# Kernel optimization log

Hardware: AMD Instinct MI355X
Metric: run time of the kernel (lower is better)

The kernel has to match this reference:

```python
import jax, jax.numpy as jnp
import numpy as np

B, H, W = 2, 512, 512
HID, NHKD, HEADS, KD, CD = 64, 128, 8, 16, 64
MAX_SHAPE = 512

def _conv(x, w, b=None, pad=0, groups=1):
    y = jax.lax.conv_general_dilated(x, w, (1, 1), [(pad, pad), (pad, pad)],
                                     dimension_numbers=('NCHW', 'OIHW', 'NCHW'),
                                     feature_group_count=groups)
    return y if b is None else y + b[None, :, None, None]

def _gelu(x):
    return jax.nn.gelu(x, approximate=False)  # torch nn.GELU default is exact erf

def _bn(x, s, t):
    # inference-mode BatchNorm folded to per-channel scale/shift
    return x * s[None, :, None, None] + t[None, :, None, None]

def _dyn_pos(xm, pe):
    # xm: (B, C, N); pe: (1, C, MAX_SHAPE); linear interp (align_corners=False) when N != MAX_SHAPE
    N = xm.shape[-1]
    if N != pe.shape[-1]:
        pe = jax.image.resize(pe, (1, pe.shape[1], N), method='linear')
    return xm + pe

def _sdpa(q, k, v):
    # q, k, v: (B, heads, L=key_dim, E=H); scale = 1/sqrt(E) as in F.scaled_dot_product_attention
    scale = 1.0 / np.sqrt(q.shape[-1])
    attn = jax.nn.softmax(jnp.einsum('bhie,bhje->bhij', q, k) * scale, axis=-1)
    return jnp.einsum('bhij,bhje->bhie', attn, v)

def setup_inputs():
    key = jax.random.key(0)
    ks = jax.random.split(key, 26)
    rn = lambda i, shp, sc=1.0: jax.random.normal(ks[i], shp, jnp.float32) * sc
    return {
        'x': rn(0, (B, HID, H, W)),
        'shortcut': rn(1, (B, CD, H, W)),
        'ln_w': jnp.ones((CD,), jnp.float32),
        'ln_b': jnp.zeros((CD,), jnp.float32),
        'dproj_dw_w': rn(2, (CD, 1, 3, 3), 0.2),
        'dproj_bn_s': 1.0 + rn(3, (CD,), 0.1),
        'dproj_bn_t': rn(4, (CD,), 0.1),
        'dproj_pw_w': rn(5, (2 * HID, CD, 1, 1), 0.125),
        'dproj_pw_b': rn(6, (2 * HID,), 0.05),
        'q_dw_w': rn(7, (NHKD, 1, 3, 3), 0.2),
        'q_bn_s': 1.0 + rn(8, (NHKD,), 0.1),
        'q_bn_t': rn(9, (NHKD,), 0.1),
        'k_dw_w': rn(10, (NHKD, 1, 3, 3), 0.2),
        'k_bn_s': 1.0 + rn(11, (NHKD,), 0.1),
        'k_bn_t': rn(12, (NHKD,), 0.1),
        'v_pw_w': rn(13, (NHKD, HID, 1, 1), 0.125),
        'v_bn_s': 1.0 + rn(14, (NHKD,), 0.1),
        'v_bn_t': rn(15, (NHKD,), 0.1),
        'proj_dw_w': rn(16, (HID + 2 * NHKD, 1, 3, 3), 0.2),
        'proj_dw_b': rn(17, (HID + 2 * NHKD,), 0.05),
        'proj_pw_w': rn(18, (HID, HID + 2 * NHKD, 1, 1), 0.06),
        'proj_pw_b': rn(19, (HID,), 0.05),
        'pe_rowq': rn(20, (1, NHKD, MAX_SHAPE), 0.02),
        'pe_rowk': rn(21, (1, NHKD, MAX_SHAPE), 0.02),
        'pe_colq': rn(22, (1, NHKD, MAX_SHAPE), 0.02),
        'pe_colk': rn(23, (1, NHKD, MAX_SHAPE), 0.02),
        'ape_row_w': jnp.ones((1, NHKD, 1, 1), jnp.float32),
        'ape_col_w': jnp.ones((1, NHKD, 1, 1), jnp.float32),
    }

def reference(x, shortcut, ln_w, ln_b, dproj_dw_w, dproj_bn_s, dproj_bn_t,
              dproj_pw_w, dproj_pw_b, q_dw_w, q_bn_s, q_bn_t, k_dw_w, k_bn_s,
              k_bn_t, v_pw_w, v_bn_s, v_bn_t, proj_dw_w, proj_dw_b, proj_pw_w,
              proj_pw_b, pe_rowq, pe_rowk, pe_colq, pe_colk, ape_row_w, ape_col_w):
    b, _, h, w = x.shape
    # LayerNorm2d: normalize over channel axis (biased variance, eps=1e-5)
    mu = shortcut.mean(axis=1, keepdims=True)
    var = shortcut.var(axis=1, keepdims=True)
    sn = (shortcut - mu) / jnp.sqrt(var + 1e-5) * ln_w[None, :, None, None] + ln_b[None, :, None, None]
    # d_proj: dw3x3 -> BN -> GELU -> pw1x1 -> GELU
    s = _gelu(_bn(_conv(sn, dproj_dw_w, pad=1, groups=CD), dproj_bn_s, dproj_bn_t))
    s = _gelu(_conv(s, dproj_pw_w, dproj_pw_b))
    k_in, v_in = jnp.split(s, 2, axis=1)  # each (B, HID, H, W)
    # q/k: grouped 3x3 conv (groups=HID, out=NHKD) -> BN -> GELU; v: 1x1 -> BN
    q = _gelu(_bn(_conv(x, q_dw_w, pad=1, groups=HID), q_bn_s, q_bn_t))
    k = _gelu(_bn(_conv(k_in, k_dw_w, pad=1, groups=HID), k_bn_s, k_bn_t))
    v = _bn(_conv(v_in, v_pw_w), v_bn_s, v_bn_t)
    # row attention: pool over W, seq dim = key_dim (16), head dim = H
    qr = _dyn_pos(q.mean(-1), pe_rowq).reshape(b, HEADS, KD, h)
    kr = _dyn_pos(k.mean(-1), pe_rowk).reshape(b, HEADS, KD, h)
    vr = v.mean(-1).reshape(b, HEADS, KD, h)
    attn_row = _sdpa(qr, kr, vr).reshape(b, NHKD, 1, h)
    # column attention: pool over H
    qc = _dyn_pos(q.mean(-2), pe_colq).reshape(b, HEADS, KD, w)
    kc = _dyn_pos(k.mean(-2), pe_colk).reshape(b, HEADS, KD, w)
    vc = v.mean(-2).reshape(b, HEADS, KD, w)
    attn_col = _sdpa(qc, kc, vc).reshape(b, NHKD, 1, w)
    # AxialPositionEncoding: both maps broadcast over spatial axis 2 (requires H == W)
    attn = v + ape_row_w * attn_row + ape_col_w * attn_col
    cat = jnp.concatenate([x, attn, v], axis=1)  # (B, 320, H, W)
    ctot = cat.shape[1]
    # channel shuffle: 'b (c g) h w -> b (g c) h w', g=5
    shuf = cat.reshape(b, ctot // 5, 5, h, w).transpose(0, 2, 1, 3, 4).reshape(b, ctot, h, w)
    p = _gelu(_conv(shuf, proj_dw_w, proj_dw_b, pad=1, groups=ctot))
    p = _conv(p, proj_pw_w, proj_pw_b)
    return _gelu(p)
```

## Files before the change

kernel.cpp:

```cpp
#include <hip/hip_runtime.h>
#include <math.h>

#define PLANE (512*512)

typedef short bf16x8 __attribute__((ext_vector_type(8)));
typedef float f32x4 __attribute__((ext_vector_type(4)));

__device__ __forceinline__ float gelu_f(float x) {
    float ax = fabsf(x) * 0.70710678118654752440f;
    float t = __builtin_amdgcn_rcpf(1.0f + 0.3275911f * ax);
    float poly = t * (0.254829592f + t * (-0.284496736f + t * (1.421413741f
               + t * (-1.453152027f + t * 1.061405429f))));
    float e = __expf(-ax * ax);
    float er = 1.0f - poly * e;
    er = copysignf(er, x);
    return 0.5f * x * (1.0f + er);
}

__device__ __forceinline__ unsigned short f2bf(float f) {
    union { float f; unsigned u; } v; v.f = f;
    unsigned r = v.u + 0x7FFFu + ((v.u >> 16) & 1u);
    return (unsigned short)(r >> 16);
}

__global__ __launch_bounds__(256) void k_lnstats(const float* __restrict__ sc,
                                                 float* __restrict__ Pb,
                                                 float* __restrict__ Qb) {
    int p = blockIdx.x * 256 + threadIdx.x;
    int b = p >> 18;
    int hw = p & (PLANE - 1);
    const float* src = sc + (size_t)b * 64 * PLANE + hw;
    float sum = 0.f, sq = 0.f;
    #pragma unroll 8
    for (int c = 0; c < 64; ++c) {
        float v = src[(size_t)c * PLANE];
        sum += v; sq += v * v;
    }
    float mu = sum * (1.0f / 64.0f);
    float var = sq * (1.0f / 64.0f) - mu * mu;
    float rstd = rsqrtf(var + 1e-5f);
    Pb[p] = rstd;
    Qb[p] = -mu * rstd;
}

__global__ __launch_bounds__(256) void k_dw64ln(const float* __restrict__ sc,
                                                const float* __restrict__ dww,
                                                const float* __restrict__ lnw,
                                                const float* __restrict__ lnb,
                                                const float* __restrict__ bns,
                                                const float* __restrict__ bnt,
                                                const float* __restrict__ Pb,
                                                const float* __restrict__ Qb,
                                                unsigned* __restrict__ t1b) {
    int p = blockIdx.x * 256 + threadIdx.x;
    int b = p >> 18;
    int hw = p & (PLANE - 1);
    int h = hw >> 9, w = hw & 511;
    int tapoff[9]; float Pt[9], Qt[9], vm[9];
    const float* Pp = Pb + (size_t)b * PLANE;
    const float* Qp = Qb + (size_t)b * PLANE;
    #pragma unroll
    for (int dh = -1; dh <= 1; ++dh)
        #pragma unroll
        for (int dw = -1; dw <= 1; ++dw) {
            int k = (dh + 1) * 3 + dw + 1;
            int hh = h + dh, ww = w + dw;
            bool ok = (hh >= 0 && hh < 512 && ww >= 0 && ww < 512);
            int hc = ok ? hh : h, wc = ok ? ww : w;
            int off = hc * 512 + wc;
            tapoff[k] = off;
            vm[k] = ok ? 1.f : 0.f;
            Pt[k] = Pp[off]; Qt[k] = Qp[off];
        }
    const float* scb = sc + (size_t)b * 64 * PLANE;
    unsigned* ob = t1b + (size_t)b * 32 * PLANE + hw;
    for (int c2 = 0; c2 < 32; ++c2) {
        float g[2];
        #pragma unroll
        for (int e = 0; e < 2; ++e) {
            int c = c2 * 2 + e;
            const float* wp = dww + c * 9;
            const float* cp = scb + (size_t)c * PLANE;
            float conv = 0.f, wsum = 0.f;
            #pragma unroll
            for (int k = 0; k < 9; ++k) {
                float wv = wp[k];
                float raw = cp[tapoff[k]];
                conv = fmaf(wv, fmaf(raw, Pt[k], Qt[k]) * vm[k], conv);
                wsum = fmaf(wv, vm[k], wsum);
            }
            float a = lnw[c] * conv + lnb[c] * wsum;
            g[e] = gelu_f(a * bns[c] + bnt[c]);
        }
        unsigned r;
        asm("v_cvt_pk_bf16_f32 %0,%1,%2" : "=v"(r) : "v"(g[0]), "v"(g[1]));
        ob[(size_t)c2 * PLANE] = r;
    }
}

__global__ __launch_bounds__(256) void k_wsetup2(const float* __restrict__ W1,
                                                 const float* __restrict__ W2,
                                                 unsigned short* __restrict__ w1b,
                                                 unsigned short* __restrict__ w2b) {
    int tid = blockIdx.x * 256 + threadIdx.x;
    if (tid < 8192) { w1b[tid] = f2bf(W1[tid]); w2b[tid] = f2bf(W2[tid]); }
}

__global__ __launch_bounds__(256, 4) void k_pw2(
    const unsigned* __restrict__ t1b,
    const unsigned short* __restrict__ w1b, const float* __restrict__ b1,
    const unsigned short* __restrict__ w2b,
    const float* __restrict__ vbs, const float* __restrict__ vbt,
    float* __restrict__ k_in, float* __restrict__ v)
{
    __shared__ unsigned short vin[64][88];
    __shared__ float epi[64 * 68];
    __shared__ float psl[128], ptl[128], pbl[128];
    int tid = threadIdx.x;
    if (tid < 128) { psl[tid] = vbs[tid]; ptl[tid] = vbt[tid]; pbl[tid] = b1[tid]; }
    int lane = tid & 63, wva = tid >> 6;
    int cl = lane & 15, kg = lane >> 4;
    int p0 = blockIdx.x * 64;
    int b = p0 >> 18;
    int hw0 = p0 & (PLANE - 1);
    int px = wva * 16 + cl;
    const unsigned* tp = t1b + (size_t)b * 32 * PLANE + hw0 + px;
    __syncthreads();

    unsigned bfr[2][4];
    #pragma unroll
    for (int ks = 0; ks < 2; ++ks)
        #pragma unroll
        for (int jp = 0; jp < 4; ++jp)
            bfr[ks][jp] = tp[(size_t)(ks * 16 + kg * 4 + jp) * PLANE];

    f32x4 acc[8];
    #pragma unroll
    for (int mt = 0; mt < 8; ++mt) acc[mt] = (f32x4){0.f, 0.f, 0.f, 0.f};
    #pragma unroll
    for (int ks = 0; ks < 2; ++ks) {
        union { unsigned u[4]; bf16x8 v; } bb;
        bb.u[0] = bfr[ks][0]; bb.u[1] = bfr[ks][1]; bb.u[2] = bfr[ks][2]; bb.u[3] = bfr[ks][3];
        #pragma unroll
        for (int mt = 0; mt < 8; ++mt) {
            bf16x8 af = *(const bf16x8*)(w1b + (size_t)(mt * 16 + cl) * 64 + ks * 32 + kg * 8);
            acc[mt] = __builtin_amdgcn_mfma_f32_16x16x32_bf16(af, bb.v, acc[mt], 0, 0, 0);
        }
    }

    #pragma unroll
    for (int mt = 4; mt < 8; ++mt) {
        float g[4];
        #pragma unroll
        for (int r = 0; r < 4; ++r)
            g[r] = gelu_f(acc[mt][r] + pbl[mt * 16 + kg * 4 + r]);
        unsigned r01, r23;
        asm("v_cvt_pk_bf16_f32 %0,%1,%2" : "=v"(r01) : "v"(g[0]), "v"(g[1]));
        asm("v_cvt_pk_bf16_f32 %0,%1,%2" : "=v"(r23) : "v"(g[2]), "v"(g[3]));
        int ch = (mt - 4) * 16 + kg * 4;
        *(unsigned*)&vin[px][ch]     = r01;
        *(unsigned*)&vin[px][ch + 2] = r23;
    }

    __syncthreads();
    #pragma unroll
    for (int mt = 0; mt < 4; ++mt)
        #pragma unroll
        for (int r = 0; r < 4; ++r) {
            int m = mt * 16 + kg * 4 + r;
            epi[m * 68 + px] = gelu_f(acc[mt][r] + pbl[m]);
        }
    __syncthreads();
    float* kb = k_in + (size_t)b * 64 * PLANE + hw0;
    #pragma unroll
    for (int k = 0; k < 4; ++k) {
        int m = wva * 16 + k * 4 + kg;
        float4 vv = *(const float4*)&epi[m * 68 + cl * 4];
        *(float4*)&kb[(size_t)m * PLANE + cl * 4] = vv;
    }

    f32x4 acc2[8];
    #pragma unroll
    for (int mt = 0; mt < 8; ++mt) acc2[mt] = (f32x4){0.f, 0.f, 0.f, 0.f};
    #pragma unroll
    for (int ks = 0; ks < 2; ++ks) {
        bf16x8 bb = *(const bf16x8*)&vin[px][ks * 32 + kg * 8];
        #pragma unroll
        for (int mt = 0; mt < 8; ++mt) {
            bf16x8 af = *(const bf16x8*)(w2b + (size_t)(mt * 16 + cl) * 64 + ks * 32 + kg * 8);
            acc2[mt] = __builtin_amdgcn_mfma_f32_16x16x32_bf16(af, bb, acc2[mt], 0, 0, 0);
        }
    }

    float* vb = v + (size_t)b * 128 * PLANE + hw0;
    #pragma unroll
    for (int pass = 0; pass < 2; ++pass) {
        __syncthreads();
        #pragma unroll
        for (int mt = pass * 4; mt < pass * 4 + 4; ++mt)
            #pragma unroll
            for (int r = 0; r < 4; ++r) {
                int m = mt * 16 + kg * 4 + r;
                epi[(m - pass * 64) * 68 + px] = acc2[mt][r] * psl[m] + ptl[m];
            }
        __syncthreads();
        #pragma unroll
        for (int k = 0; k < 4; ++k) {
            int ml = wva * 16 + k * 4 + kg;
            float4 vv = *(const float4*)&epi[ml * 68 + cl * 4];
            *(float4*)&vb[(size_t)(pass * 64 + ml) * PLANE + cl * 4] = vv;
        }
    }
}

__global__ __launch_bounds__(512) void k_dwpool(const float* __restrict__ in,
                                                const float* __restrict__ wt,
                                                const float* __restrict__ bns,
                                                const float* __restrict__ bnt,
                                                float* __restrict__ rowsum,
                                                float* __restrict__ colpart) {
    __shared__ float lred[2][8][8];
    int tid = threadIdx.x;
    int blk = blockIdx.x;
    int hc = blk & 63;
    int g  = (blk >> 6) & 63;
    int b  = blk >> 12;
    int o0 = 2 * g, o1 = 2 * g + 1;
    const float* ip = in + ((size_t)b * 64 + g) * PLANE;
    float w0[9], w1[9];
    #pragma unroll
    for (int k = 0; k < 9; ++k) { w0[k] = wt[o0 * 9 + k]; w1[k] = wt[o1 * 9 + k]; }
    float s0 = bns[o0], t0 = bnt[o0], s1 = bns[o1], tt1 = bnt[o1];
    int wx = tid;
    float ca0 = 0.f, ca1 = 0.f;
    int lane = tid & 63, wv = tid >> 6;
    for (int r = 0; r < 8; ++r) {
        int h = hc * 8 + r;
        float nb[9];
        #pragma unroll
        for (int dh = -1; dh <= 1; ++dh) {
            #pragma unroll
            for (int dw = -1; dw <= 1; ++dw) {
                int hh = h + dh, ww = wx + dw;
                nb[(dh + 1) * 3 + dw + 1] =
                    (hh >= 0 && hh < 512 && ww >= 0 && ww < 512) ? ip[hh * 512 + ww] : 0.f;
            }
        }
        float a0 = 0.f, a1 = 0.f;
        #pragma unroll
        for (int k = 0; k < 9; ++k) { a0 += w0[k] * nb[k]; a1 += w1[k] * nb[k]; }
        a0 = gelu_f(a0 * s0 + t0);
        a1 = gelu_f(a1 * s1 + tt1);
        ca0 += a0; ca1 += a1;
        #pragma unroll
        for (int off = 32; off > 0; off >>= 1) {
            a0 += __shfl_down(a0, off, 64);
            a1 += __shfl_down(a1, off, 64);
        }
        if (lane == 0) { lred[0][r][wv] = a0; lred[1][r][wv] = a1; }
    }
    colpart[(((size_t)b * 128 + o0) * 64 + hc) * 512 + wx] = ca0;
    colpart[(((size_t)b * 128 + o1) * 64 + hc) * 512 + wx] = ca1;
    __syncthreads();
    if (tid < 16) {
        int oo = tid >> 3, r = tid & 7;
        float s = 0.f;
        #pragma unroll
        for (int i = 0; i < 8; ++i) s += lred[oo][r][i];
        int och = oo == 0 ? o0 : o1;
        rowsum[((size_t)b * 128 + och) * 512 + hc * 8 + r] = s;
    }
}

__global__ __launch_bounds__(512) void k_vpool(const float* __restrict__ v,
                                               float* __restrict__ rowsum,
                                               float* __restrict__ colpart) {
    __shared__ float lred[8][8];
    int tid = threadIdx.x;
    int blk = blockIdx.x;
    int hc = blk & 63;
    int bc = blk >> 6;
    const float* ip = v + (size_t)bc * PLANE;
    float ca = 0.f;
    int lane = tid & 63, wv = tid >> 6;
    for (int r = 0; r < 8; ++r) {
        float a = ip[(hc * 8 + r) * 512 + tid];
        ca += a;
        #pragma unroll
        for (int off = 32; off > 0; off >>= 1) a += __shfl_down(a, off, 64);
        if (lane == 0) lred[r][wv] = a;
    }
    colpart[((size_t)bc * 64 + hc) * 512 + tid] = ca;
    __syncthreads();
    if (tid < 8) {
        float s = 0.f;
        #pragma unroll
        for (int i = 0; i < 8; ++i) s += lred[tid][i];
        rowsum[(size_t)bc * 512 + hc * 8 + tid] = s;
    }
}

__global__ __launch_bounds__(256) void k_colreduce(const float* __restrict__ part,
                                                   float* __restrict__ out, int n) {
    int idx = blockIdx.x * 256 + threadIdx.x;
    if (idx >= n) return;
    int bc = idx >> 9, w = idx & 511;
    const float* pp = part + ((size_t)bc * 64) * 512 + w;
    float s = 0.f;
    #pragma unroll
    for (int p = 0; p < 64; ++p) s += pp[p * 512];
    out[idx] = s;
}

__global__ __launch_bounds__(256) void k_attn(const float* __restrict__ qrow,
                                              const float* __restrict__ krow,
                                              const float* __restrict__ vrow,
                                              const float* __restrict__ qcol,
                                              const float* __restrict__ kcol,
                                              const float* __restrict__ vcol,
                                              const float* __restrict__ perq,
                                              const float* __restrict__ perk,
                                              const float* __restrict__ pecq,
                                              const float* __restrict__ peck,
                                              float* __restrict__ arow,
                                              float* __restrict__ acol) {
    __shared__ float P[16][17];
    int blk = blockIdx.x;
    int axis = blk & 1;
    int head = (blk >> 1) & 7;
    int b = blk >> 4;
    const float* qs = axis ? qcol : qrow;
    const float* ks = axis ? kcol : krow;
    const float* vs = axis ? vcol : vrow;
    const float* peq = axis ? pecq : perq;
    const float* pek = axis ? peck : perk;
    float* out = axis ? acol : arow;
    int tid = threadIdx.x;
    int i = tid >> 4, j = tid & 15;
    int ci = head * 16 + i, cj = head * 16 + j;
    const float* qp = qs + ((size_t)b * 128 + ci) * 512;
    const float* kp = ks + ((size_t)b * 128 + cj) * 512;
    const float* qe = peq + ci * 512;
    const float* ke = pek + cj * 512;
    float s = 0.f;
    for (int n = 0; n < 512; ++n) {
        float qv = qp[n] * (1.f / 512.f) + qe[n];
        float kv = kp[n] * (1.f / 512.f) + ke[n];
        s += qv * kv;
    }
    s *= 0.0441941738241592203f;
    P[i][j] = s;
    __syncthreads();
    if (tid < 16) {
        float mx = -1e30f;
        #pragma unroll
        for (int jj = 0; jj < 16; ++jj) mx = fmaxf(mx, P[tid][jj]);
        float e[16];
        float sum = 0.f;
        #pragma unroll
        for (int jj = 0; jj < 16; ++jj) { e[jj] = expf(P[tid][jj] - mx); sum += e[jj]; }
        float inv = 1.f / sum;
        #pragma unroll
        for (int jj = 0; jj < 16; ++jj) P[tid][jj] = e[jj] * inv;
    }
    __syncthreads();
    for (int idx = tid; idx < 16 * 512; idx += 256) {
        int ii = idx >> 9, n = idx & 511;
        const float* vb = vs + ((size_t)b * 128 + head * 16) * 512 + n;
        float acc = 0.f;
        #pragma unroll
        for (int jj = 0; jj < 16; ++jj) acc += P[ii][jj] * vb[jj * 512] * (1.f / 512.f);
        out[((size_t)b * 128 + head * 16 + ii) * 512 + n] = acc;
    }
}

__global__ __launch_bounds__(256) void k_wsetup(const float* __restrict__ pww,
                                                unsigned short* __restrict__ wsh) {
    int tid = blockIdx.x * 256 + threadIdx.x;
    if (tid >= 64 * 320) return;
    int m = tid / 320, src = tid % 320;
    int o = (src % 5) * 64 + src / 5;
    wsh[m * 320 + src] = f2bf(pww[m * 320 + o]);
}

__global__ __launch_bounds__(256) void k_awsetup(const float* __restrict__ pdw,
                                                 const float* __restrict__ aprw,
                                                 const float* __restrict__ apcw,
                                                 const float* __restrict__ arow,
                                                 const float* __restrict__ acol,
                                                 float* __restrict__ aw) {
    int idx = blockIdx.x * 256 + threadIdx.x;
    if (idx >= 2 * 128 * 512) return;
    int col = idx & 511;
    int c   = (idx >> 9) & 127;
    int b   = idx >> 16;
    int src = 64 + c;
    int o = (src % 5) * 64 + src / 5;
    const float* wd = pdw + o * 9;
    float ws0 = wd[0] + wd[3] + wd[6];
    float ws1 = wd[1] + wd[4] + wd[7];
    float ws2 = wd[2] + wd[5] + wd[8];
    const float* ar = arow + ((size_t)b * 128 + c) * 512;
    const float* ac = acol + ((size_t)b * 128 + c) * 512;
    float apr = aprw[c], apc = apcw[c];
    float sum = ws1 * (apr * ar[col] + apc * ac[col]);
    if (col > 0)   sum += ws0 * (apr * ar[col - 1] + apc * ac[col - 1]);
    if (col < 511) sum += ws2 * (apr * ar[col + 1] + apc * ac[col + 1]);
    aw[idx] = sum;
}

template<bool HE, bool WE>
__device__ __forceinline__ void conv2x2(const float* __restrict__ p,
    const float* wlA, const float* wlP,
    const int* hrow, const float* rv, int ls, int rs, float cv0, float cv2,
    float outA[2], float outP[2])
{
    float a0,a1,a2, b0,b1,b2, c0,c1,c2;
    const float* q = p + hrow[0]*512;
    if (WE) { a0=q[ls]*cv0; a1=q[0]; a2=q[rs]*cv2; } else { a0=q[-1]; a1=q[0]; a2=q[1]; }
    q = p + hrow[1]*512;
    if (WE) { b0=q[ls]*cv0; b1=q[0]; b2=q[rs]*cv2; } else { b0=q[-1]; b1=q[0]; b2=q[1]; }
    q = p + hrow[2]*512;
    if (WE) { c0=q[ls]*cv0; c1=q[0]; c2=q[rs]*cv2; } else { c0=q[-1]; c1=q[0]; c2=q[1]; }
    #pragma unroll
    for (int hs = 0; hs < 2; ++hs) {
        float sA0 = wlA[0]*a0 + wlA[1]*a1 + wlA[2]*a2;
        float sA1 = wlA[3]*b0 + wlA[4]*b1 + wlA[5]*b2;
        float sA2 = wlA[6]*c0 + wlA[7]*c1 + wlA[8]*c2;
        float sP0 = wlP[0]*a0 + wlP[1]*a1 + wlP[2]*a2;
        float sP1 = wlP[3]*b0 + wlP[4]*b1 + wlP[5]*b2;
        float sP2 = wlP[6]*c0 + wlP[7]*c1 + wlP[8]*c2;
        if (HE) {
            outA[hs] = rv[hs]*sA0 + sA1 + rv[hs+2]*sA2 + wlA[9];
            outP[hs] = rv[hs]*sP0 + sP1 + rv[hs+2]*sP2 + wlP[9];
        } else {
            outA[hs] = sA0 + sA1 + sA2 + wlA[9];
            outP[hs] = sP0 + sP1 + sP2 + wlP[9];
        }
        if (hs < 1) {
            a0=b0; a1=b1; a2=b2; b0=c0; b1=c1; b2=c2;
            q = p + hrow[3]*512;
            if (WE) { c0=q[ls]*cv0; c1=q[0]; c2=q[rs]*cv2; } else { c0=q[-1]; c1=q[0]; c2=q[1]; }
        }
    }
}

template<bool HE, bool WE>
__device__ __forceinline__ void conv1x2(const float* __restrict__ p,
    const float* wl,
    const int* hrow, const float* rv, int ls, int rs, float cv0, float cv2,
    float out[2])
{
    float a0,a1,a2, b0,b1,b2, c0,c1,c2;
    const float* q = p + hrow[0]*512;
    if (WE) { a0=q[ls]*cv0; a1=q[0]; a2=q[rs]*cv2; } else { a0=q[-1]; a1=q[0]; a2=q[1]; }
    q = p + hrow[1]*512;
    if (WE) { b0=q[ls]*cv0; b1=q[0]; b2=q[rs]*cv2; } else { b0=q[-1]; b1=q[0]; b2=q[1]; }
    q = p + hrow[2]*512;
    if (WE) { c0=q[ls]*cv0; c1=q[0]; c2=q[rs]*cv2; } else { c0=q[-1]; c1=q[0]; c2=q[1]; }
    #pragma unroll
    for (int hs = 0; hs < 2; ++hs) {
        float s0 = wl[0]*a0 + wl[1]*a1 + wl[2]*a2;
        float s1 = wl[3]*b0 + wl[4]*b1 + wl[5]*b2;
        float s2 = wl[6]*c0 + wl[7]*c1 + wl[8]*c2;
        out[hs] = (HE ? (rv[hs]*s0 + s1 + rv[hs+2]*s2) : (s0 + s1 + s2)) + wl[9];
        if (hs < 1) {
            a0=b0; a1=b1; a2=b2; b0=c0; b1=c1; b2=c2;
            q = p + hrow[3]*512;
            if (WE) { c0=q[ls]*cv0; c1=q[0]; c2=q[rs]*cv2; } else { c0=q[-1]; c1=q[0]; c2=q[1]; }
        }
    }
}

template<bool HE, bool WE>
__device__ __forceinline__ void proj5_core(
    int h0, int wwbase, float* epi, const float* dwl,
    const float* __restrict__ xb, const float* __restrict__ vbp,
    const float* __restrict__ arb, const float* __restrict__ acb,
    const float* __restrict__ aprw, const float* __restrict__ apcw,
    const float* __restrict__ awb,
    const unsigned short* __restrict__ wsh, const float* __restrict__ pwb,
    float* __restrict__ outb)
{
    int tid = threadIdx.x;
    int lane = tid & 63, wva = tid >> 6;
    int cl = lane & 15, kg = lane >> 4;
    int ww = wwbase + wva * 16 + cl;

    int hrow[4]; float rv[4];
    #pragma unroll
    for (int i = 0; i < 4; ++i) {
        int r = h0 - 1 + i;
        float va = 1.f;
        if (HE) { if (r < 0) { r = 0; va = 0.f; } if (r > 511) { r = 511; va = 0.f; } }
        hrow[i] = r; rv[i] = va;
    }
    int ls = -1, rs = 1; float cv0 = 1.f, cv2 = 1.f;
    if (WE) {
        if (ww == 0)   { ls = 1;  cv0 = 0.f; }
        if (ww == 511) { rs = -1; cv2 = 0.f; }
    }

    f32x4 acc[2][4];
    #pragma unroll
    for (int hs = 0; hs < 2; ++hs)
        #pragma unroll
        for (int mt = 0; mt < 4; ++mt)
            acc[hs][mt] = (f32x4){0.f, 0.f, 0.f, 0.f};

    #pragma unroll
    for (int ks = 0; ks < 2; ++ks) {
        unsigned bp[2][4];
        #pragma unroll
        for (int jp = 0; jp < 4; ++jp) {
            float cj0[2], cj1[2];
            int ch = ks * 32 + kg * 8 + jp * 2;
            conv1x2<HE,WE>(xb + (size_t)ch * PLANE + ww, dwl + ch * 12,
                           hrow, rv, ls, rs, cv0, cv2, cj0);
            conv1x2<HE,WE>(xb + (size_t)(ch+1) * PLANE + ww, dwl + (ch+1) * 12,
                           hrow, rv, ls, rs, cv0, cv2, cj1);
            #pragma unroll
            for (int hs = 0; hs < 2; ++hs) {
                float g0 = gelu_f(cj0[hs]), g1 = gelu_f(cj1[hs]);
                unsigned r;
                asm("v_cvt_pk_bf16_f32 %0,%1,%2" : "=v"(r) : "v"(g0), "v"(g1));
                bp[hs][jp] = r;
            }
        }
        #pragma unroll
        for (int mt = 0; mt < 4; ++mt) {
            bf16x8 af = *(const bf16x8*)(wsh + (size_t)(mt * 16 + cl) * 320 + ks * 32 + kg * 8);
            #pragma unroll
            for (int hs = 0; hs < 2; ++hs) {
                union { unsigned u[4]; bf16x8 v; } bb;
                bb.u[0] = bp[hs][0]; bb.u[1] = bp[hs][1]; bb.u[2] = bp[hs][2]; bb.u[3] = bp[hs][3];
                acc[hs][mt] = __builtin_amdgcn_mfma_f32_16x16x32_bf16(af, bb.v, acc[hs][mt], 0, 0, 0);
            }
        }
    }

    #pragma unroll
    for (int vks = 0; vks < 4; ++vks) {
        unsigned bpA[2][4], bpP[2][4];
        #pragma unroll
        for (int jp = 0; jp < 4; ++jp) {
            float cA[2][2], cP[2][2];
            #pragma unroll
            for (int e = 0; e < 2; ++e) {
                int c = vks * 32 + kg * 8 + jp * 2 + e;
                const float* wlA = dwl + (64 + c) * 12;
                conv2x2<HE,WE>(vbp + (size_t)c * PLANE + ww, wlA, dwl + (192 + c) * 12,
                               hrow, rv, ls, rs, cv0, cv2, cA[e], cP[e]);
                float awv = awb[(size_t)c * 512 + ww];
                #pragma unroll
                for (int hs = 0; hs < 2; ++hs) {
                    if (!HE) {
                        cA[e][hs] += awv;
                    } else {
                        if (rv[hs] + rv[hs + 2] == 2.f) {
                            cA[e][hs] += awv;
                        } else {
                            const float* arp = arb + (size_t)c * 512 + ww;
                            const float* acp = acb + (size_t)c * 512 + ww;
                            float apr = aprw[c], apc = apcw[c];
                            float aa0 = (apr * arp[ls] + apc * acp[ls]) * cv0;
                            float aa1 =  apr * arp[0]  + apc * acp[0];
                            float aa2 = (apr * arp[rs] + apc * acp[rs]) * cv2;
                            float wd0 = rv[hs]*wlA[0] + wlA[3] + rv[hs+2]*wlA[6];
                            float wd1 = rv[hs]*wlA[1] + wlA[4] + rv[hs+2]*wlA[7];
                            float wd2 = rv[hs]*wlA[2] + wlA[5] + rv[hs+2]*wlA[8];
                            cA[e][hs] += wd0*aa0 + wd1*aa1 + wd2*aa2;
                        }
                    }
                }
            }
            #pragma unroll
            for (int hs = 0; hs < 2; ++hs) {
                float gA0 = gelu_f(cA[0][hs]), gA1 = gelu_f(cA[1][hs]);
                float gP0 = gelu_f(cP[0][hs]), gP1 = gelu_f(cP[1][hs]);
                unsigned ra, rp;
                asm("v_cvt_pk_bf16_f32 %0,%1,%2" : "=v"(ra) : "v"(gA0), "v"(gA1));
                asm("v_cvt_pk_bf16_f32 %0,%1,%2" : "=v"(rp) : "v"(gP0), "v"(gP1));
                bpA[hs][jp] = ra; bpP[hs][jp] = rp;
            }
        }
        #pragma unroll
        for (int mt = 0; mt < 4; ++mt) {
            bf16x8 afA = *(const bf16x8*)(wsh + (size_t)(mt * 16 + cl) * 320 + (2 + vks) * 32 + kg * 8);
            #pragma unroll
            for (int hs = 0; hs < 2; ++hs) {
                union { unsigned u[4]; bf16x8 v; } bb;
                bb.u[0] = bpA[hs][0]; bb.u[1] = bpA[hs][1]; bb.u[2] = bpA[hs][2]; bb.u[3] = bpA[hs][3];
                acc[hs][mt] = __builtin_amdgcn_mfma_f32_16x16x32_bf16(afA, bb.v, acc[hs][mt], 0, 0, 0);
            }
            bf16x8 afP = *(const bf16x8*)(wsh + (size_t)(mt * 16 + cl) * 320 + (6 + vks) * 32 + kg * 8);
            #pragma unroll
            for (int hs = 0; hs < 2; ++hs) {
                union { unsigned u[4]; bf16x8 v; } bb;
                bb.u[0] = bpP[hs][0]; bb.u[1] = bpP[hs][1]; bb.u[2] = bpP[hs][2]; bb.u[3] = bpP[hs][3];
                acc[hs][mt] = __builtin_amdgcn_mfma_f32_16x16x32_bf16(afP, bb.v, acc[hs][mt], 0, 0, 0);
            }
        }
    }

    #pragma unroll
    for (int hs = 0; hs < 2; ++hs) {
        __syncthreads();
        #pragma unroll
        for (int mt = 0; mt < 4; ++mt)
            #pragma unroll
            for (int r = 0; r < 4; ++r) {
                int m = mt * 16 + kg * 4 + r;
                epi[m * 68 + wva * 16 + cl] = gelu_f(acc[hs][mt][r] + pwb[m]);
            }
        __syncthreads();
        #pragma unroll
        for (int k = 0; k < 4; ++k) {
            int m = wva * 16 + k * 4 + kg;
            float4 vv = *(const float4*)&epi[m * 68 + cl * 4];
            *(float4*)&outb[(size_t)m * PLANE + (size_t)(h0 + hs) * 512 + wwbase + cl * 4] = vv;
        }
    }
}

__global__ __launch_bounds__(256, 4) void k_proj5(
    const float* __restrict__ x, const float* __restrict__ v,
    const float* __restrict__ arow, const float* __restrict__ acol,
    const float* __restrict__ aprw, const float* __restrict__ apcw,
    const float* __restrict__ dww, const float* __restrict__ dwb,
    const unsigned short* __restrict__ wsh, const float* __restrict__ pwb,
    const float* __restrict__ aw, float* __restrict__ out)
{
    __shared__ float dwl[320 * 12];
    __shared__ float epi[64 * 68];
    int tid = threadIdx.x;
    for (int i = tid; i < 3200; i += 256) {
        int src = i / 10, k = i - src * 10;
        int o = (src % 5) * 64 + src / 5;
        dwl[src * 12 + k] = (k < 9) ? dww[o * 9 + k] : dwb[o];
    }
    __syncthreads();
    int flat = blockIdx.x;
    int nf = (flat & 7) * 512 + (flat >> 3);
    int bx = nf & 7;
    int s  = (nf >> 3) & 255;
    int b  = nf >> 11;
    int h0 = s * 2, wwbase = bx * 64;
    const float* xb  = x + (size_t)b * 64 * PLANE;
    const float* vbp = v + (size_t)b * 128 * PLANE;
    const float* arb = arow + (size_t)b * 128 * 512;
    const float* acb = acol + (size_t)b * 128 * 512;
    const float* awb = aw + (size_t)b * 128 * 512;
    float* outb = out + (size_t)b * 64 * PLANE;
    bool HEr = (s == 0) || (s == 255);
    bool WEr = (bx == 0) || (bx == 7);
    if (!HEr && !WEr)
        proj5_core<false,false>(h0, wwbase, epi, dwl, xb, vbp, arb, acb, aprw, apcw, awb, wsh, pwb, outb);
    else if (!HEr)
        proj5_core<false,true >(h0, wwbase, epi, dwl, xb, vbp, arb, acb, aprw, apcw, awb, wsh, pwb, outb);
    else
        proj5_core<true ,true >(h0, wwbase, epi, dwl, xb, vbp, arb, acb, aprw, apcw, awb, wsh, pwb, outb);
}

extern "C" void kernel_launch(void* const* d_in, const int* in_sizes, int n_in,
                              void* d_out, int out_size, void* d_ws, size_t ws_size,
                              hipStream_t stream) {
    const float* x    = (const float*)d_in[0];
    const float* sc   = (const float*)d_in[1];
    const float* lnw  = (const float*)d_in[2];
    const float* lnb  = (const float*)d_in[3];
    const float* ddw  = (const float*)d_in[4];
    const float* dbs  = (const float*)d_in[5];
    const float* dbt  = (const float*)d_in[6];
    const float* pw1  = (const float*)d_in[7];
    const float* pb1  = (const float*)d_in[8];
    const float* qdw  = (const float*)d_in[9];
    const float* qbs  = (const float*)d_in[10];
    const float* qbt  = (const float*)d_in[11];
    const float* kdw  = (const float*)d_in[12];
    const float* kbs  = (const float*)d_in[13];
    const float* kbt  = (const float*)d_in[14];
    const float* vpw  = (const float*)d_in[15];
    const float* vbs  = (const float*)d_in[16];
    const float* vbt  = (const float*)d_in[17];
    const float* pdw  = (const float*)d_in[18];
    const float* pdb  = (const float*)d_in[19];
    const float* ppw  = (const float*)d_in[20];
    const float* ppb  = (const float*)d_in[21];
    const float* perq = (const float*)d_in[22];
    const float* perk = (const float*)d_in[23];
    const float* pecq = (const float*)d_in[24];
    const float* peck = (const float*)d_in[25];
    const float* aprw = (const float*)d_in[26];
    const float* apcw = (const float*)d_in[27];

    float* bufA = (float*)d_out;
    float* ws   = (float*)d_ws;
    float* bufB = ws;
    float* bufV = ws + 33554432;
    float* sm   = ws + 100663296;
    float* qrow = sm;
    float* krow = sm + 131072;
    float* vrow = sm + 262144;
    float* qcol = sm + 393216;
    float* kcol = sm + 524288;
    float* vcol = sm + 655360;
    float* arow = sm + 786432;
    float* acol = sm + 917504;
    unsigned short* wsh = (unsigned short*)(ws + 101711872);
    float* aw   = ws + 101722112;
    unsigned short* w1b = (unsigned short*)(ws + 101853184);
    unsigned short* w2b = (unsigned short*)(ws + 101857280);
    float* Pb   = ws + 101861376;
    float* Qb   = ws + 102385664;
    unsigned* t1b = (unsigned*)bufB;
    float* qcp  = bufB;
    float* kcp  = bufB + 8388608;
    float* vcp  = bufB + 16777216;

    k_wsetup <<<80,   256, 0, stream>>>(ppw, wsh);
    k_wsetup2<<<32,   256, 0, stream>>>(pw1, vpw, w1b, w2b);
    k_lnstats<<<2048, 256, 0, stream>>>(sc, Pb, Qb);
    k_dw64ln <<<2048, 256, 0, stream>>>(sc, ddw, lnw, lnb, dbs, dbt, Pb, Qb, t1b);
    k_pw2    <<<8192, 256, 0, stream>>>(t1b, w1b, pb1, w2b, vbs, vbt, bufA, bufV);
    k_dwpool <<<8192, 512, 0, stream>>>(x,    qdw, qbs, qbt, qrow, qcp);
    k_dwpool <<<8192, 512, 0, stream>>>(bufA, kdw, kbs, kbt, krow, kcp);
    k_vpool  <<<16384,512, 0, stream>>>(bufV, vrow, vcp);
    k_colreduce<<<1536,256, 0, stream>>>(qcp, qcol, 393216);
    k_attn   <<<32,   256, 0, stream>>>(qrow, krow, vrow, qcol, kcol, vcol,
                                        perq, perk, pecq, peck, arow, acol);
    k_awsetup<<<512,  256, 0, stream>>>(pdw, aprw, apcw, arow, acol, aw);
    k_proj5  <<<4096, 256, 0, stream>>>(x, bufV, arow, acol, aprw, apcw,
                                        pdw, pdb, wsh, ppb, aw, (float*)d_out);
}
```

Measured before the change: 1.038 ms.

## Fuse LN depthwise conv into pointwise MFMA kernel and preload weights

Removes the separate k_dw64ln kernel: the LayerNorm-folded depthwise 3x3 conv plus GELU is now computed inside the pointwise MFMA kernel (k_pw3), straight into bf16 B-fragment registers. This avoids writing and re-reading the intermediate t1b buffer, at the cost of more per-thread work and register pressure ahead of the MFMAs. Per-channel BN/LN scales are folded into a shared-memory table, and the proj kernel now loads depthwise weights as vectors into registers. The q dwpool launch is also moved after the v pool.

```diff
diff --git a/kernel.cpp b/kernel.cpp
--- a/kernel.cpp
+++ b/kernel.cpp
@@ -21,6 +21,15 @@
     union { float f; unsigned u; } v; v.f = f;
     unsigned r = v.u + 0x7FFFu + ((v.u >> 16) & 1u);
     return (unsigned short)(r >> 16);
+}
+
+__device__ __forceinline__ void ldw(const float* p, float wk[10]) {
+    f32x4 a = *(const f32x4*)p;
+    f32x4 b = *(const f32x4*)(p + 4);
+    f32x4 c = *(const f32x4*)(p + 8);
+    wk[0]=a[0]; wk[1]=a[1]; wk[2]=a[2]; wk[3]=a[3];
+    wk[4]=b[0]; wk[5]=b[1]; wk[6]=b[2]; wk[7]=b[3];
+    wk[8]=c[0]; wk[9]=c[1];
 }
 
 __global__ __launch_bounds__(256) void k_lnstats(const float* __restrict__ sc,
@@ -43,61 +52,6 @@
     Qb[p] = -mu * rstd;
 }
 
-__global__ __launch_bounds__(256) void k_dw64ln(const float* __restrict__ sc,
-                                                const float* __restrict__ dww,
-                                                const float* __restrict__ lnw,
-                                                const float* __restrict__ lnb,
-                                                const float* __restrict__ bns,
-                                                const float* __restrict__ bnt,
-                                                const float* __restrict__ Pb,
-                                                const float* __restrict__ Qb,
-                                                unsigned* __restrict__ t1b) {
-    int p = blockIdx.x * 256 + threadIdx.x;
-    int b = p >> 18;
-    int hw = p & (PLANE - 1);
-    int h = hw >> 9, w = hw & 511;
-    int tapoff[9]; float Pt[9], Qt[9], vm[9];
-    const float* Pp = Pb + (size_t)b * PLANE;
-    const float* Qp = Qb + (size_t)b * PLANE;
-    #pragma unroll
-    for (int dh = -1; dh <= 1; ++dh)
-        #pragma unroll
-        for (int dw = -1; dw <= 1; ++dw) {
-            int k = (dh + 1) * 3 + dw + 1;
-            int hh = h + dh, ww = w + dw;
-            bool ok = (hh >= 0 && hh < 512 && ww >= 0 && ww < 512);
-            int hc = ok ? hh : h, wc = ok ? ww : w;
-            int off = hc * 512 + wc;
-            tapoff[k] = off;
-            vm[k] = ok ? 1.f : 0.f;
-            Pt[k] = Pp[off]; Qt[k] = Qp[off];
-        }
-    const float* scb = sc + (size_t)b * 64 * PLANE;
-    unsigned* ob = t1b + (size_t)b * 32 * PLANE + hw;
-    for (int c2 = 0; c2 < 32; ++c2) {
-        float g[2];
-        #pragma unroll
-        for (int e = 0; e < 2; ++e) {
-            int c = c2 * 2 + e;
-            const float* wp = dww + c * 9;
-            const float* cp = scb + (size_t)c * PLANE;
-            float conv = 0.f, wsum = 0.f;
-            #pragma unroll
-            for (int k = 0; k < 9; ++k) {
-                float wv = wp[k];
-                float raw = cp[tapoff[k]];
-                conv = fmaf(wv, fmaf(raw, Pt[k], Qt[k]) * vm[k], conv);
-                wsum = fmaf(wv, vm[k], wsum);
-            }
-            float a = lnw[c] * conv + lnb[c] * wsum;
-            g[e] = gelu_f(a * bns[c] + bnt[c]);
-        }
-        unsigned r;
-        asm("v_cvt_pk_bf16_f32 %0,%1,%2" : "=v"(r) : "v"(g[0]), "v"(g[1]));
-        ob[(size_t)c2 * PLANE] = r;
-    }
-}
-
 __global__ __launch_bounds__(256) void k_wsetup2(const float* __restrict__ W1,
                                                  const float* __restrict__ W2,
                                                  unsigned short* __restrict__ w1b,
@@ -106,33 +60,87 @@
     if (tid < 8192) { w1b[tid] = f2bf(W1[tid]); w2b[tid] = f2bf(W2[tid]); }
 }
 
-__global__ __launch_bounds__(256, 4) void k_pw2(
-    const unsigned* __restrict__ t1b,
+__global__ __launch_bounds__(256, 4) void k_pw3(
+    const float* __restrict__ sc,
+    const float* __restrict__ dww,
+    const float* __restrict__ lnw, const float* __restrict__ lnb,
+    const float* __restrict__ bns, const float* __restrict__ bnt,
+    const float* __restrict__ Pb, const float* __restrict__ Qb,
     const unsigned short* __restrict__ w1b, const float* __restrict__ b1,
     const unsigned short* __restrict__ w2b,
     const float* __restrict__ vbs, const float* __restrict__ vbt,
     float* __restrict__ k_in, float* __restrict__ v)
 {
+    __shared__ float prm[64 * 12];
     __shared__ unsigned short vin[64][88];
     __shared__ float epi[64 * 68];
     __shared__ float psl[128], ptl[128], pbl[128];
     int tid = threadIdx.x;
     if (tid < 128) { psl[tid] = vbs[tid]; ptl[tid] = vbt[tid]; pbl[tid] = b1[tid]; }
+    for (int i = tid; i < 64 * 12; i += 256) {
+        int c = i / 12, k = i - c * 12;
+        float val;
+        if (k < 9)       val = dww[c * 9 + k];
+        else if (k == 9) val = lnw[c] * bns[c];
+        else if (k == 10)val = lnb[c] * bns[c];
+        else             val = bnt[c];
+        prm[i] = val;
+    }
     int lane = tid & 63, wva = tid >> 6;
     int cl = lane & 15, kg = lane >> 4;
     int p0 = blockIdx.x * 64;
     int b = p0 >> 18;
     int hw0 = p0 & (PLANE - 1);
+    int h = hw0 >> 9, w0 = hw0 & 511;
     int px = wva * 16 + cl;
-    const unsigned* tp = t1b + (size_t)b * 32 * PLANE + hw0 + px;
+    int w = w0 + px;
+    int tapoff[9]; float Pt[9], Qt[9], vm[9];
+    const float* Pp = Pb + (size_t)b * PLANE;
+    const float* Qp = Qb + (size_t)b * PLANE;
+    #pragma unroll
+    for (int dh = -1; dh <= 1; ++dh)
+        #pragma unroll
+        for (int dw2 = -1; dw2 <= 1; ++dw2) {
+            int k = (dh + 1) * 3 + dw2 + 1;
+            int hh = h + dh, ww = w + dw2;
+            bool ok = (hh >= 0 && hh < 512 && ww >= 0 && ww < 512);
+            int hc = ok ? hh : h, wc = ok ? ww : w;
+            int off = hc * 512 + wc;
+            tapoff[k] = off; vm[k] = ok ? 1.f : 0.f;
+            Pt[k] = Pp[off]; Qt[k] = Qp[off];
+        }
     __syncthreads();
+    const float* scb = sc + (size_t)b * 64 * PLANE;
 
     unsigned bfr[2][4];
     #pragma unroll
     for (int ks = 0; ks < 2; ++ks)
         #pragma unroll
-        for (int jp = 0; jp < 4; ++jp)
-            bfr[ks][jp] = tp[(size_t)(ks * 16 + kg * 4 + jp) * PLANE];
+        for (int jp = 0; jp < 4; ++jp) {
+            float g2[2];
+            #pragma unroll
+            for (int e = 0; e < 2; ++e) {
+                int c = ks * 32 + kg * 8 + jp * 2 + e;
+                const float* pr = prm + c * 12;
+                f32x4 wv0 = *(const f32x4*)pr;
+                f32x4 wv1 = *(const f32x4*)(pr + 4);
+                f32x4 wv2 = *(const f32x4*)(pr + 8);
+                float wk[9] = {wv0[0],wv0[1],wv0[2],wv0[3],wv1[0],wv1[1],wv1[2],wv1[3],wv2[0]};
+                const float* cp = scb + (size_t)c * PLANE;
+                float conv = 0.f, wsum = 0.f;
+                #pragma unroll
+                for (int k = 0; k < 9; ++k) {
+                    float t = fmaf(cp[tapoff[k]], Pt[k], Qt[k]) * vm[k];
+                    conv = fmaf(wk[k], t, conv);
+                    wsum = fmaf(wk[k], vm[k], wsum);
+                }
+                float a = wv2[1] * conv + wv2[2] * wsum + wv2[3];
+                g2[e] = gelu_f(a);
+            }
+            unsigned r;
+            asm("v_cvt_pk_bf16_f32 %0,%1,%2" : "=v"(r) : "v"(g2[0]), "v"(g2[1]));
+            bfr[ks][jp] = r;
+        }
 
     f32x4 acc[8];
     #pragma unroll
@@ -515,9 +523,12 @@
         for (int jp = 0; jp < 4; ++jp) {
             float cj0[2], cj1[2];
             int ch = ks * 32 + kg * 8 + jp * 2;
-            conv1x2<HE,WE>(xb + (size_t)ch * PLANE + ww, dwl + ch * 12,
+            float wk0[10], wk1[10];
+            ldw(dwl + ch * 12, wk0);
+            ldw(dwl + (ch + 1) * 12, wk1);
+            conv1x2<HE,WE>(xb + (size_t)ch * PLANE + ww, wk0,
                            hrow, rv, ls, rs, cv0, cv2, cj0);
-            conv1x2<HE,WE>(xb + (size_t)(ch+1) * PLANE + ww, dwl + (ch+1) * 12,
+            conv1x2<HE,WE>(xb + (size_t)(ch+1) * PLANE + ww, wk1,
                            hrow, rv, ls, rs, cv0, cv2, cj1);
             #pragma unroll
             for (int hs = 0; hs < 2; ++hs) {
@@ -548,8 +559,10 @@
             #pragma unroll
             for (int e = 0; e < 2; ++e) {
                 int c = vks * 32 + kg * 8 + jp * 2 + e;
-                const float* wlA = dwl + (64 + c) * 12;
-                conv2x2<HE,WE>(vbp + (size_t)c * PLANE + ww, wlA, dwl + (192 + c) * 12,
+                float wkA[10], wkP[10];
+                ldw(dwl + (64 + c) * 12, wkA);
+                ldw(dwl + (192 + c) * 12, wkP);
+                conv2x2<HE,WE>(vbp + (size_t)c * PLANE + ww, wkA, wkP,
                                hrow, rv, ls, rs, cv0, cv2, cA[e], cP[e]);
                 float awv = awb[(size_t)c * 512 + ww];
                 #pragma unroll
@@ -566,9 +579,9 @@
                             float aa0 = (apr * arp[ls] + apc * acp[ls]) * cv0;
                             float aa1 =  apr * arp[0]  + apc * acp[0];
                             float aa2 = (apr * arp[rs] + apc * acp[rs]) * cv2;
-                            float wd0 = rv[hs]*wlA[0] + wlA[3] + rv[hs+2]*wlA[6];
-                            float wd1 = rv[hs]*wlA[1] + wlA[4] + rv[hs+2]*wlA[7];
-                            float wd2 = rv[hs]*wlA[2] + wlA[5] + rv[hs+2]*wlA[8];
+                            float wd0 = rv[hs]*wkA[0] + wkA[3] + rv[hs+2]*wkA[6];
+                            float wd1 = rv[hs]*wkA[1] + wkA[4] + rv[hs+2]*wkA[7];
+                            float wd2 = rv[hs]*wkA[2] + wkA[5] + rv[hs+2]*wkA[8];
                             cA[e][hs] += wd0*aa0 + wd1*aa1 + wd2*aa2;
                         }
                     }
@@ -713,7 +726,6 @@
     unsigned short* w2b = (unsigned short*)(ws + 101857280);
     float* Pb   = ws + 101861376;
     float* Qb   = ws + 102385664;
-    unsigned* t1b = (unsigned*)bufB;
     float* qcp  = bufB;
     float* kcp  = bufB + 8388608;
     float* vcp  = bufB + 16777216;
@@ -721,11 +733,11 @@
     k_wsetup <<<80,   256, 0, stream>>>(ppw, wsh);
     k_wsetup2<<<32,   256, 0, stream>>>(pw1, vpw, w1b, w2b);
     k_lnstats<<<2048, 256, 0, stream>>>(sc, Pb, Qb);
-    k_dw64ln <<<2048, 256, 0, stream>>>(sc, ddw, lnw, lnb, dbs, dbt, Pb, Qb, t1b);
-    k_pw2    <<<8192, 256, 0, stream>>>(t1b, w1b, pb1, w2b, vbs, vbt, bufA, bufV);
-    k_dwpool <<<8192, 512, 0, stream>>>(x,    qdw, qbs, qbt, qrow, qcp);
+    k_pw3    <<<8192, 256, 0, stream>>>(sc, ddw, lnw, lnb, dbs, dbt, Pb, Qb,
+                                        w1b, pb1, w2b, vbs, vbt, bufA, bufV);
     k_dwpool <<<8192, 512, 0, stream>>>(bufA, kdw, kbs, kbt, krow, kcp);
     k_vpool  <<<16384,512, 0, stream>>>(bufV, vrow, vcp);
+    k_dwpool <<<8192, 512, 0, stream>>>(x,    qdw, qbs, qbt, qrow, qcp);
     k_colreduce<<<1536,256, 0, stream>>>(qcp, qcol, 393216);
     k_attn   <<<32,   256, 0, stream>>>(qrow, krow, vrow, qcol, kcol, vcol,
                                         perq, perk, pecq, peck, arow, acol);
```

Result: slower. 1.065 ms (+2.5%).
